# Kernel tuning notes

Hardware: AMD Instinct MI355X
Metric: run time of the kernel (lower is better)

The kernel has to match this reference:

```python
import jax, jax.numpy as jnp
import numpy as np

B, N, D = 2, 2048, 768
H = 12
HD = D // H
HID = 4 * D
SCALE = HD ** -0.5
EPS = 1e-5


def layer_norm(x, g, b):
    mu = jnp.mean(x, axis=-1, keepdims=True)
    var = jnp.var(x, axis=-1, keepdims=True)
    return (x - mu) * jax.lax.rsqrt(var + EPS) * g + b


def setup_inputs() -> dict:
    key = jax.random.key(0)
    ks = jax.random.split(key, 12)
    s = 0.02
    return {
        "x": jax.random.normal(ks[0], (B, N, D), jnp.float32),
        "att_mask": jax.random.randint(ks[1], (B, N), 0, 2, jnp.int32),
        "ln1_g": jnp.ones((D,), jnp.float32),
        "ln1_b": jnp.zeros((D,), jnp.float32),
        "qkv_w": jax.random.normal(ks[2], (3 * D, D), jnp.float32) * s,
        "q_bias": jnp.zeros((D,), jnp.float32),
        "v_bias": jnp.zeros((D,), jnp.float32),
        "proj_w": jax.random.normal(ks[3], (D, D), jnp.float32) * s,
        "proj_b": jnp.zeros((D,), jnp.float32),
        "ln2_g": jnp.ones((D,), jnp.float32),
        "ln2_b": jnp.zeros((D,), jnp.float32),
        "fc1_w": jax.random.normal(ks[4], (HID, D), jnp.float32) * s,
        "fc1_b": jnp.zeros((HID,), jnp.float32),
        "fc2_w": jax.random.normal(ks[5], (D, HID), jnp.float32) * s,
        "fc2_b": jnp.zeros((D,), jnp.float32),
        "gamma_1": 0.1 * jnp.ones((D,), jnp.float32),
        "gamma_2": 0.1 * jnp.ones((D,), jnp.float32),
    }


def reference(x, att_mask, ln1_g, ln1_b, qkv_w, q_bias, v_bias, proj_w, proj_b,
              ln2_g, ln2_b, fc1_w, fc1_b, fc2_w, fc2_b, gamma_1, gamma_2):
    # --- attention branch ---
    h = layer_norm(x, ln1_g, ln1_b)
    qkv_bias = jnp.concatenate([q_bias, jnp.zeros_like(v_bias), v_bias])
    qkv = h @ qkv_w.T + qkv_bias                      # [B,N,3D]
    qkv = qkv.reshape(B, N, 3, H, HD).transpose(2, 0, 3, 1, 4)
    q, k, v = qkv[0], qkv[1], qkv[2]                  # [B,H,N,HD]
    logit = jnp.einsum('bhqd,bhkd->bhqk', q * SCALE, k)
    mask = att_mask[:, None, None, :]                 # key mask [B,1,1,N]
    logit = jnp.where(mask == 0, -jnp.inf, logit)
    attn = jax.nn.softmax(logit, axis=-1)
    o = jnp.einsum('bhqk,bhkd->bhqd', attn, v)
    o = o.transpose(0, 2, 1, 3).reshape(B, N, D)
    o = o @ proj_w.T + proj_b
    x = x + gamma_1 * o
    # --- mlp branch ---
    h2 = layer_norm(x, ln2_g, ln2_b)
    h2 = jax.nn.gelu(h2 @ fc1_w.T + fc1_b, approximate=False)
    h2 = h2 @ fc2_w.T + fc2_b
    return x + gamma_2 * h2
```

## Files before the change

### kernel.cpp

```cpp
#include <hip/hip_runtime.h>
#include <hip/hip_bf16.h>
#include <stdint.h>

typedef __bf16 bf16x8 __attribute__((ext_vector_type(8)));
typedef unsigned short u16x8 __attribute__((ext_vector_type(8)));
typedef float f32x4 __attribute__((ext_vector_type(4)));
typedef float f32x16 __attribute__((ext_vector_type(16)));
typedef uint32_t u32x4 __attribute__((ext_vector_type(4)));

#define DMODEL 768
#define NSEQ   2048
#define BATCH  2
#define NHEAD  12
#define HDIM   64
#define HIDDEN 3072
#define PROWS  (BATCH * NHEAD * NSEQ)
#define QSCALE 0.18033688011112042f

__device__ __forceinline__ uint16_t f2bf(float f) {
  __hip_bfloat16 h = __float2bfloat16(f);
  return __builtin_bit_cast(uint16_t, h);
}
__device__ __forceinline__ float bf2f(uint16_t u) {
  uint32_t x = (uint32_t)u << 16;
  return __builtin_bit_cast(float, x);
}
__device__ __forceinline__ bf16x8 ldb8(const uint16_t* p) {
  return __builtin_bit_cast(bf16x8, *reinterpret_cast<const u16x8*>(p));
}

using as1_void = __attribute__((address_space(1))) const void;
using as3_void = __attribute__((address_space(3))) void;
__device__ __forceinline__ void gload16(const uint16_t* src, uint16_t* lds) {
  __builtin_amdgcn_global_load_lds((as1_void*)src, (as3_void*)lds, 16, 0, 0);
}
#define MEMFENCE asm volatile("" ::: "memory")

#define N_QKVW  (3 * DMODEL * DMODEL)
#define N_PROJW (DMODEL * DMODEL)
#define N_FC1W  (HIDDEN * DMODEL)
#define N_FC2W  (DMODEL * HIDDEN)
__global__ __launch_bounds__(256) void cvt4_kernel(const float* __restrict__ s0,
                                                   const float* __restrict__ s1,
                                                   const float* __restrict__ s2,
                                                   const float* __restrict__ s3,
                                                   uint16_t* __restrict__ d0,
                                                   uint16_t* __restrict__ d1,
                                                   uint16_t* __restrict__ d2,
                                                   uint16_t* __restrict__ d3) {
  int i4 = (blockIdx.x * 256 + threadIdx.x) * 4;
  const float* s;
  uint16_t* d;
  if (i4 < N_QKVW) { s = s0 + i4; d = d0 + i4; }
  else if (i4 < N_QKVW + N_PROJW) { int j = i4 - N_QKVW; s = s1 + j; d = d1 + j; }
  else if (i4 < N_QKVW + N_PROJW + N_FC1W) { int j = i4 - N_QKVW - N_PROJW; s = s2 + j; d = d2 + j; }
  else { int j = i4 - N_QKVW - N_PROJW - N_FC1W; s = s3 + j; d = d3 + j; }
  float4 v = *reinterpret_cast<const float4*>(s);
  ushort4 o;
  o.x = f2bf(v.x); o.y = f2bf(v.y); o.z = f2bf(v.z); o.w = f2bf(v.w);
  *reinterpret_cast<ushort4*>(d) = o;
}

__global__ __launch_bounds__(256) void bias_kernel(const float* __restrict__ qb,
                                                   const float* __restrict__ vb,
                                                   float* __restrict__ out) {
  int j = blockIdx.x * 256 + threadIdx.x;
  if (j < 3 * DMODEL) {
    float v = 0.f;
    if (j < DMODEL) v = qb[j];
    else if (j >= 2 * DMODEL) v = vb[j - 2 * DMODEL];
    out[j] = v;
  }
}

__global__ __launch_bounds__(256) void ln_kernel(const float* __restrict__ x,
                                                 const float* __restrict__ g,
                                                 const float* __restrict__ bt,
                                                 uint16_t* __restrict__ out) {
  const int row = blockIdx.x;
  const int t = threadIdx.x;
  const float* xr = x + (size_t)row * DMODEL;
  float v0 = xr[t], v1 = xr[t + 256], v2 = xr[t + 512];
  float s = v0 + v1 + v2;
  float q = v0 * v0 + v1 * v1 + v2 * v2;
  for (int off = 32; off >= 1; off >>= 1) {
    s += __shfl_xor(s, off);
    q += __shfl_xor(q, off);
  }
  __shared__ float ss[4], sq[4];
  int w = t >> 6;
  if ((t & 63) == 0) { ss[w] = s; sq[w] = q; }
  __syncthreads();
  s = ss[0] + ss[1] + ss[2] + ss[3];
  q = sq[0] + sq[1] + sq[2] + sq[3];
  const float mean = s * (1.0f / DMODEL);
  const float var = q * (1.0f / DMODEL) - mean * mean;
  const float rstd = rsqrtf(var + 1e-5f);
  uint16_t* orow = out + (size_t)row * DMODEL;
  orow[t]       = f2bf((v0 - mean) * rstd * g[t]       + bt[t]);
  orow[t + 256] = f2bf((v1 - mean) * rstd * g[t + 256] + bt[t + 256]);
  orow[t + 512] = f2bf((v2 - mean) * rstd * g[t + 512] + bt[t + 512]);
}

template <int MODE>
__global__ __launch_bounds__(256, 3) void gemm128(const uint16_t* __restrict__ A,
                                                  const uint16_t* __restrict__ W,
                                                  const float* __restrict__ bias,
                                                  void* __restrict__ outp,
                                                  int M, int N, int K) {
  __shared__ uint16_t As[2][128 * 32];
  __shared__ uint16_t Bs[2][128 * 32];
  const int tid = threadIdx.x;
  const int lane = tid & 63;
  const int w = tid >> 6;
  const int wr = w >> 1, wc = w & 1;
  const int row0 = blockIdx.y * 128;
  const int col0 = blockIdx.x * 128;
  const int lr = lane & 15;
  const int g = lane >> 4;

  const int o0 = w * 1024 + lane * 16;
  const int o1 = o0 + 4096;
  const int r0s = o0 >> 6, c0s = (o0 & 63) >> 1;
  const int r1s = o1 >> 6, c1s = (o1 & 63) >> 1;
  const int l0 = (w * 1024) >> 1;
  const int l1 = l0 + 2048;
  const uint16_t* Abase = A + (size_t)row0 * K;
  const uint16_t* Wbase = W + (size_t)col0 * K;

  auto stage = [&](int kt) {
    uint16_t* Ad = &As[kt & 1][0];
    uint16_t* Bd = &Bs[kt & 1][0];
    const int kk = kt * 32;
    gload16(Abase + (size_t)r0s * K + kk + c0s, Ad + l0);
    gload16(Abase + (size_t)r1s * K + kk + c1s, Ad + l1);
    gload16(Wbase + (size_t)r0s * K + kk + c0s, Bd + l0);
    gload16(Wbase + (size_t)r1s * K + kk + c1s, Bd + l1);
  };

  f32x4 acc[4][4] = {};
  const int nt = K >> 5;
  stage(0);
  for (int kt = 0; kt < nt; ++kt) {
    if (kt + 1 < nt) {
      stage(kt + 1);
      asm volatile("s_waitcnt vmcnt(4)" ::: "memory");
    } else {
      asm volatile("s_waitcnt vmcnt(0)" ::: "memory");
    }
    __builtin_amdgcn_s_barrier();
    MEMFENCE;
    const uint16_t* Ab = &As[kt & 1][0];
    const uint16_t* Bb = &Bs[kt & 1][0];
    bf16x8 a[4], b[4];
#pragma unroll
    for (int m = 0; m < 4; ++m) a[m] = ldb8(Ab + (wr * 64 + m * 16 + lr) * 32 + g * 8);
#pragma unroll
    for (int n = 0; n < 4; ++n) b[n] = ldb8(Bb + (wc * 64 + n * 16 + lr) * 32 + g * 8);
#pragma unroll
    for (int m = 0; m < 4; ++m)
#pragma unroll
      for (int n = 0; n < 4; ++n)
        acc[m][n] = __builtin_amdgcn_mfma_f32_16x16x32_bf16(a[m], b[n], acc[m][n], 0, 0, 0);
    MEMFENCE;
    __builtin_amdgcn_s_barrier();
  }

#pragma unroll
  for (int m = 0; m < 4; ++m) {
    int row = row0 + wr * 64 + m * 16 + g * 4;
#pragma unroll
    for (int n = 0; n < 4; ++n) {
      int col = col0 + wc * 64 + n * 16 + lr;
      float bv = bias[col];
#pragma unroll
      for (int ri = 0; ri < 4; ++ri) {
        float val = acc[m][n][ri] + bv;
        size_t idx = (size_t)(row + ri) * N + col;
        if constexpr (MODE == 0) {
          if (col < DMODEL) val *= QSCALE;
          ((uint16_t*)outp)[idx] = f2bf(val);
        } else {
          float ge = 0.5f * val * (1.0f + erff(val * 0.70710678118654752f));
          ((uint16_t*)outp)[idx] = f2bf(ge);
        }
      }
    }
  }
}

__global__ __launch_bounds__(128, 2) void gemm64(const uint16_t* __restrict__ A,
                                                 const uint16_t* __restrict__ W,
                                                 const float* __restrict__ bias,
                                                 float* __restrict__ outp,
                                                 const float* __restrict__ resid,
                                                 const float* __restrict__ gamma,
                                                 int M, int N, int K) {
  __shared__ uint16_t As[2][64 * 32];
  __shared__ uint16_t Bs[2][64 * 32];
  const int tid = threadIdx.x;
  const int lane = tid & 63;
  const int wv = tid >> 6;
  const int row0 = blockIdx.y * 64;
  const int col0 = blockIdx.x * 64;
  const int lr = lane & 15;
  const int g = lane >> 4;
  const int rs = tid >> 2;
  const int cs = (tid & 3) * 8;
  const uint16_t* Abase = A + (size_t)row0 * K;
  const uint16_t* Wbase = W + (size_t)col0 * K;

  auto stage = [&](int kt) {
    uint16_t* Ad = &As[kt & 1][0];
    uint16_t* Bd = &Bs[kt & 1][0];
    const int kk = kt * 32;
#pragma unroll
    for (int i = 0; i < 2; ++i) {
      gload16(Abase + (size_t)(i * 32 + rs) * K + kk + cs, Ad + i * 1024 + wv * 512);
      gload16(Wbase + (size_t)(i * 32 + rs) * K + kk + cs, Bd + i * 1024 + wv * 512);
    }
  };

  f32x4 acc[4][2] = {};
  const int nt = K >> 5;
  stage(0);
  for (int kt = 0; kt < nt; ++kt) {
    if (kt + 1 < nt) {
      stage(kt + 1);
      asm volatile("s_waitcnt vmcnt(4)" ::: "memory");
    } else {
      asm volatile("s_waitcnt vmcnt(0)" ::: "memory");
    }
    __builtin_amdgcn_s_barrier();
    MEMFENCE;
    const uint16_t* Ab = &As[kt & 1][0];
    const uint16_t* Bb = &Bs[kt & 1][0];
    bf16x8 a[4], b[2];
#pragma unroll
    for (int m = 0; m < 4; ++m) a[m] = ldb8(Ab + (m * 16 + lr) * 32 + g * 8);
#pragma unroll
    for (int n = 0; n < 2; ++n) b[n] = ldb8(Bb + (wv * 32 + n * 16 + lr) * 32 + g * 8);
#pragma unroll
    for (int m = 0; m < 4; ++m)
#pragma unroll
      for (int n = 0; n < 2; ++n)
        acc[m][n] = __builtin_amdgcn_mfma_f32_16x16x32_bf16(a[m], b[n], acc[m][n], 0, 0, 0);
    MEMFENCE;
    __builtin_amdgcn_s_barrier();
  }

#pragma unroll
  for (int m = 0; m < 4; ++m) {
    int row = row0 + m * 16 + g * 4;
#pragma unroll
    for (int n = 0; n < 2; ++n) {
      int col = col0 + wv * 32 + n * 16 + lr;
      float bv = bias[col];
      float gv = gamma[col];
#pragma unroll
      for (int ri = 0; ri < 4; ++ri) {
        float val = acc[m][n][ri] + bv;
        size_t idx = (size_t)(row + ri) * N + col;
        outp[idx] = resid[idx] + gv * val;
      }
    }
  }
}

__global__ __launch_bounds__(256) void prep_kernel(const uint16_t* __restrict__ qkv,
                                                   const int* __restrict__ mask,
                                                   uint16_t* __restrict__ km,
                                                   uint16_t* __restrict__ vt) {
  __shared__ uint16_t tile[64][72];
  const int t = threadIdx.x;
  const int bh = blockIdx.x;
  const int n0 = blockIdx.y * 64;
  const int b = bh / NHEAD, h = bh % NHEAD;
  const int* mb = mask + b * NSEQ;
  const uint16_t* src = qkv + (size_t)(b * NSEQ + n0) * (3 * DMODEL) + h * HDIM;
  uint16_t* kdst = km + (size_t)(b * NSEQ + n0) * DMODEL + h * HDIM;
#pragma unroll
  for (int it = 0; it < 2; ++it) {
    int slot = it * 256 + t;
    int r = slot >> 2, c = (slot & 3) * 16;
    uint16_t mz = (mb[n0 + r] != 0) ? (uint16_t)0xFFFF : (uint16_t)0;
    const uint16_t* rp = src + (size_t)r * (3 * DMODEL);
    u16x8 k0 = *reinterpret_cast<const u16x8*>(rp + DMODEL + c) & mz;
    u16x8 k1 = *reinterpret_cast<const u16x8*>(rp + DMODEL + c + 8) & mz;
    u16x8 v0 = *reinterpret_cast<const u16x8*>(rp + 2 * DMODEL + c) & mz;
    u16x8 v1 = *reinterpret_cast<const u16x8*>(rp + 2 * DMODEL + c + 8) & mz;
    *reinterpret_cast<u16x8*>(kdst + (size_t)r * DMODEL + c) = k0;
    *reinterpret_cast<u16x8*>(kdst + (size_t)r * DMODEL + c + 8) = k1;
    *reinterpret_cast<u16x8*>(&tile[r][c]) = v0;
    *reinterpret_cast<u16x8*>(&tile[r][c + 8]) = v1;
  }
  __syncthreads();
  uint16_t* dst = vt + (size_t)bh * HDIM * NSEQ + n0;
#pragma unroll
  for (int it = 0; it < 2; ++it) {
    int slot = it * 256 + t;
    int d = slot >> 2, c = (slot & 3) * 16;
    u16x8 a0, a1;
#pragma unroll
    for (int e = 0; e < 8; ++e) a0[e] = tile[c + e][d];
#pragma unroll
    for (int e = 0; e < 8; ++e) a1[e] = tile[c + 8 + e][d];
    *reinterpret_cast<u16x8*>(dst + (size_t)d * NSEQ + c) = a0;
    *reinterpret_cast<u16x8*>(dst + (size_t)d * NSEQ + c + 8) = a1;
  }
}

__global__ __launch_bounds__(256, 3) void attn_kernel(const uint16_t* __restrict__ qkv,
                                                      const uint16_t* __restrict__ km,
                                                      const uint16_t* __restrict__ vt,
                                                      const int* __restrict__ mask,
                                                      uint16_t* __restrict__ po,
                                                      float* __restrict__ pml) {
  __shared__ uint16_t Kb[2][64 * 64];
  __shared__ uint16_t Vb[2][64 * 64];
  __shared__ unsigned long long mbits[16];
  const int tid = threadIdx.x;
  const int lane = tid & 63;
  const int w = tid >> 6;
  const int bh = blockIdx.x;
  const int b = bh / NHEAD, hd = bh % NHEAD;
  const int z = blockIdx.z;
  const int kbase = z * 1024;
  const int q0 = blockIdx.y * 128 + w * 32;
  const int l31 = lane & 31;
  const int hh = lane >> 5;

  const int* mb = mask + b * NSEQ;
#pragma unroll
  for (int it = 0; it < 4; ++it) {
    unsigned long long bm = __ballot(mb[kbase + it * 256 + tid] != 0);
    if (lane == 0) mbits[it * 4 + w] = bm;
  }

  bf16x8 qa[4];
  const uint16_t* qptr = qkv + (size_t)(b * NSEQ + q0 + l31) * (3 * DMODEL) + hd * HDIM + hh * 8;
#pragma unroll
  for (int dblk = 0; dblk < 4; ++dblk) qa[dblk] = ldb8(qptr + dblk * 16);

  const uint16_t* kmb = km + (size_t)b * NSEQ * DMODEL + hd * HDIM;
  const uint16_t* vtb = vt + (size_t)bh * HDIM * NSEQ;

  __syncthreads();

  const int srow = tid >> 3;
  const int sxor = ((tid & 7) ^ (srow & 7)) * 8;
  auto stage = [&](int t) {
    const int pb = t & 1;
    const int k0 = kbase + t * 64;
#pragma unroll
    for (int i = 0; i < 2; ++i) {
      const int row = i * 32 + srow;
      gload16(kmb + (size_t)(k0 + row) * DMODEL + sxor, &Kb[pb][i * 2048 + w * 512]);
      gload16(vtb + (size_t)row * NSEQ + k0 + sxor, &Vb[pb][i * 2048 + w * 512]);
    }
  };

  float m_ = 0.f, lsum = 0.f;
  f32x16 oacc[2] = {};

  stage(0);
  for (int t = 0; t < 16; ++t) {
    if (t + 1 < 16) {
      stage(t + 1);
      asm volatile("s_waitcnt vmcnt(4)" ::: "memory");
    } else {
      asm volatile("s_waitcnt vmcnt(0)" ::: "memory");
    }
    __builtin_amdgcn_s_barrier();
    MEMFENCE;
    const uint16_t* Kbp = &Kb[t & 1][0];
    const uint16_t* Vbp = &Vb[t & 1][0];

    f32x16 st[2];
    __builtin_amdgcn_s_setprio(1);
#pragma unroll
    for (int kblk = 0; kblk < 2; ++kblk) {
      f32x16 acc = {};
      const uint16_t* kr = Kbp + (kblk * 32 + l31) * 64;
#pragma unroll
      for (int dblk = 0; dblk < 4; ++dblk) {
        bf16x8 kf = ldb8(kr + ((dblk * 2 + hh) ^ (l31 & 7)) * 8);
        acc = __builtin_amdgcn_mfma_f32_32x32x16_bf16(kf, qa[dblk], acc, 0, 0, 0);
      }
      st[kblk] = acc;
    }
    __builtin_amdgcn_s_setprio(0);

    float tm = -1e30f;
#pragma unroll
    for (int kblk = 0; kblk < 2; ++kblk)
#pragma unroll
      for (int r = 0; r < 16; ++r) tm = fmaxf(tm, st[kblk][r]);
    tm = fmaxf(tm, __shfl_xor(tm, 32));
    if (__any(tm - m_ > 16.0f)) {
      float mn = fmaxf(m_, tm);
      float al = exp2f(m_ - mn);
      lsum *= al;
      m_ = mn;
      float ar[16];
#pragma unroll
      for (int r = 0; r < 16; ++r)
        ar[r] = __shfl(al, (r & 3) + 8 * (r >> 2) + 4 * hh);
#pragma unroll
      for (int dblk = 0; dblk < 2; ++dblk)
#pragma unroll
        for (int r = 0; r < 16; ++r) oacc[dblk][r] *= ar[r];
    }

    float ls = 0.f;
    uint32_t pk[2][8];
#pragma unroll
    for (int kblk = 0; kblk < 2; ++kblk)
#pragma unroll
      for (int wn = 0; wn < 8; ++wn) {
        float e0 = exp2f(st[kblk][2 * wn] - m_);
        float e1 = exp2f(st[kblk][2 * wn + 1] - m_);
        ls += e0 + e1;
        pk[kblk][wn] = (uint32_t)f2bf(e0) | ((uint32_t)f2bf(e1) << 16);
      }
    ls += __shfl_xor(ls, 32);
    const unsigned long long wb = mbits[t];
    const float cnt = (float)(64 - __popcll(wb));
    ls -= cnt * exp2f(0.f - m_);
    lsum += ls;

    bf16x8 af[4];
#pragma unroll
    for (int kb16 = 0; kb16 < 4; ++kb16) {
      const int kblk = kb16 >> 1;
      const int a4 = (kb16 & 1) * 4;
      uint32_t ow0 = hh ? pk[kblk][a4 + 2] : pk[kblk][a4 + 0];
      uint32_t ow1 = hh ? pk[kblk][a4 + 3] : pk[kblk][a4 + 1];
      uint32_t gv0 = hh ? pk[kblk][a4 + 0] : pk[kblk][a4 + 2];
      uint32_t gv1 = hh ? pk[kblk][a4 + 1] : pk[kblk][a4 + 3];
      uint32_t sw0 = (uint32_t)__shfl_xor((int)gv0, 32);
      uint32_t sw1 = (uint32_t)__shfl_xor((int)gv1, 32);
      u32x4 afu;
      afu[0] = hh ? sw0 : ow0;
      afu[1] = hh ? sw1 : ow1;
      afu[2] = hh ? ow0 : sw0;
      afu[3] = hh ? ow1 : sw1;
      af[kb16] = __builtin_bit_cast(bf16x8, afu);
    }

    __builtin_amdgcn_s_setprio(1);
#pragma unroll
    for (int dblk = 0; dblk < 2; ++dblk) {
      const uint16_t* vr = Vbp + (dblk * 32 + l31) * 64;
#pragma unroll
      for (int kb16 = 0; kb16 < 4; ++kb16) {
        bf16x8 vf = ldb8(vr + ((kb16 * 2 + hh) ^ (l31 & 7)) * 8);
        oacc[dblk] = __builtin_amdgcn_mfma_f32_32x32x16_bf16(af[kb16], vf, oacc[dblk], 0, 0, 0);
      }
    }
    __builtin_amdgcn_s_setprio(0);
    MEMFENCE;
    __builtin_amdgcn_s_barrier();
  }

  uint16_t* ob = po + ((size_t)z * PROWS + (size_t)bh * NSEQ + q0) * 64;
#pragma unroll
  for (int r = 0; r < 16; ++r) {
    const int qrow = (r & 3) + 8 * (r >> 2) + 4 * hh;
#pragma unroll
    for (int dblk = 0; dblk < 2; ++dblk)
      ob[(size_t)qrow * 64 + dblk * 32 + l31] = f2bf(oacc[dblk][r]);
  }
  if (hh == 0) {
    float2* pp = (float2*)(pml + ((size_t)z * PROWS + (size_t)bh * NSEQ + q0 + l31) * 2);
    *pp = make_float2(m_, lsum);
  }
}

__global__ __launch_bounds__(256) void merge_kernel(const uint16_t* __restrict__ po,
                                                    const float* __restrict__ pml,
                                                    uint16_t* __restrict__ o) {
  int gid = blockIdx.x * 256 + threadIdx.x;
  int row = gid >> 3;
  int c0 = (gid & 7) * 8;
  float m1 = pml[(size_t)row * 2], l1 = pml[(size_t)row * 2 + 1];
  float m2 = pml[((size_t)PROWS + row) * 2], l2 = pml[((size_t)PROWS + row) * 2 + 1];
  float M = fmaxf(m1, m2);
  float w1 = exp2f(m1 - M), w2 = exp2f(m2 - M);
  float L = w1 * l1 + w2 * l2;
  float inv = L > 0.f ? 1.f / L : 0.f;
  w1 *= inv; w2 *= inv;
  u16x8 a = *reinterpret_cast<const u16x8*>(po + (size_t)row * 64 + c0);
  u16x8 b = *reinterpret_cast<const u16x8*>(po + ((size_t)PROWS + row) * 64 + c0);
  int bh = row >> 11, q = row & 2047;
  int bb = bh / NHEAD, hh = bh % NHEAD;
  uint16_t* op = o + ((size_t)(bb * NSEQ + q) * DMODEL + hh * HDIM + c0);
  u16x8 outv;
#pragma unroll
  for (int e = 0; e < 8; ++e)
    outv[e] = f2bf(w1 * bf2f(a[e]) + w2 * bf2f(b[e]));
  *reinterpret_cast<u16x8*>(op) = outv;
}

extern "C" void kernel_launch(void* const* d_in, const int* in_sizes, int n_in,
                              void* d_out, int out_size, void* d_ws, size_t ws_size,
                              hipStream_t stream) {
  const float* x      = (const float*)d_in[0];
  const int*   amask  = (const int*)d_in[1];
  const float* ln1_g  = (const float*)d_in[2];
  const float* ln1_b  = (const float*)d_in[3];
  const float* qkv_w  = (const float*)d_in[4];
  const float* q_bias = (const float*)d_in[5];
  const float* v_bias = (const float*)d_in[6];
  const float* proj_w = (const float*)d_in[7];
  const float* proj_b = (const float*)d_in[8];
  const float* ln2_g  = (const float*)d_in[9];
  const float* ln2_b  = (const float*)d_in[10];
  const float* fc1_w  = (const float*)d_in[11];
  const float* fc1_b  = (const float*)d_in[12];
  const float* fc2_w  = (const float*)d_in[13];
  const float* fc2_b  = (const float*)d_in[14];
  const float* g1     = (const float*)d_in[15];
  const float* g2     = (const float*)d_in[16];

  char* ws = (char*)d_ws;
  uint16_t* qkvw_bf  = (uint16_t*)(ws + 0);
  uint16_t* projw_bf = (uint16_t*)(ws + 3538944);
  uint16_t* fc1w_bf  = (uint16_t*)(ws + 4718592);
  uint16_t* fc2w_bf  = (uint16_t*)(ws + 9437184);
  float*    qkvbias  = (float*)(ws + 14155776);
  uint16_t* h_bf     = (uint16_t*)(ws + 14164992);
  uint16_t* km       = h_bf;
  uint16_t* h2_bf    = h_bf;
  uint16_t* qkv_bf   = (uint16_t*)(ws + 20456448);
  uint16_t* vt_bf    = (uint16_t*)(ws + 39330816);
  uint16_t* o_bf     = (uint16_t*)(ws + 45622272);
  float*    x1_f     = (float*)(ws + 51913728);
  uint16_t* po       = (uint16_t*)(ws + 51913728);
  float*    pml      = (float*)(ws + 64496640);
  uint16_t* fc1_bf   = qkv_bf;

  const int M = BATCH * NSEQ;

  cvt4_kernel<<<(N_QKVW + N_PROJW + N_FC1W + N_FC2W) / 1024, 256, 0, stream>>>(
      qkv_w, proj_w, fc1_w, fc2_w, qkvw_bf, projw_bf, fc1w_bf, fc2w_bf);
  bias_kernel<<<(3 * DMODEL + 255) / 256, 256, 0, stream>>>(q_bias, v_bias, qkvbias);

  ln_kernel<<<M, 256, 0, stream>>>(x, ln1_g, ln1_b, h_bf);
  gemm128<0><<<dim3((3 * DMODEL) / 128, M / 128), 256, 0, stream>>>(
      h_bf, qkvw_bf, qkvbias, qkv_bf, M, 3 * DMODEL, DMODEL);
  prep_kernel<<<dim3(BATCH * NHEAD, NSEQ / 64), 256, 0, stream>>>(qkv_bf, amask, km, vt_bf);
  attn_kernel<<<dim3(BATCH * NHEAD, NSEQ / 128, 2), 256, 0, stream>>>(
      qkv_bf, km, vt_bf, amask, po, pml);
  merge_kernel<<<(PROWS * 8) / 256, 256, 0, stream>>>(po, pml, o_bf);
  gemm64<<<dim3(DMODEL / 64, M / 64), 128, 0, stream>>>(
      o_bf, projw_bf, proj_b, x1_f, x, g1, M, DMODEL, DMODEL);
  ln_kernel<<<M, 256, 0, stream>>>(x1_f, ln2_g, ln2_b, h2_bf);
  gemm128<2><<<dim3(HIDDEN / 128, M / 128), 256, 0, stream>>>(
      h2_bf, fc1w_bf, fc1_b, fc1_bf, M, HIDDEN, DMODEL);
  gemm64<<<dim3(DMODEL / 64, M / 64), 128, 0, stream>>>(
      fc1_bf, fc2w_bf, fc2_b, (float*)d_out, x1_f, g2, M, DMODEL, HIDDEN);
}
```

Measured before the change: 222.2 us.

## Restructure gemm64 to 4 waves with K=64 swizzled tiles; compute softmax rowsum via MFMA

The 64x64 output GEMM now uses 256 threads (a 2x2 wave grid) with a K tile of 64 and XOR-swizzled shared-memory rows, which halves the number of loop iterations and barriers and aims to reduce LDS bank conflicts. Separately, the attention kernel stops summing softmax probabilities with scalar adds and cross-lane shuffles. It instead accumulates the row sums with an extra MFMA against a vector of ones and applies the mask correction at the end. This adds MFMA work and a per-row shuffle epilogue, and the row sum is now taken from the bf16-rounded probabilities.

```diff
diff --git a/kernel.cpp b/kernel.cpp
--- a/kernel.cpp
+++ b/kernel.cpp
@@ -189,40 +189,44 @@
   }
 }
 
-__global__ __launch_bounds__(128, 2) void gemm64(const uint16_t* __restrict__ A,
+__global__ __launch_bounds__(256, 3) void gemm64(const uint16_t* __restrict__ A,
                                                  const uint16_t* __restrict__ W,
                                                  const float* __restrict__ bias,
                                                  float* __restrict__ outp,
                                                  const float* __restrict__ resid,
                                                  const float* __restrict__ gamma,
                                                  int M, int N, int K) {
-  __shared__ uint16_t As[2][64 * 32];
-  __shared__ uint16_t Bs[2][64 * 32];
+  __shared__ uint16_t As[2][64 * 64];
+  __shared__ uint16_t Bs[2][64 * 64];
   const int tid = threadIdx.x;
   const int lane = tid & 63;
-  const int wv = tid >> 6;
+  const int w = tid >> 6;
+  const int wr = w >> 1, wc = w & 1;
   const int row0 = blockIdx.y * 64;
   const int col0 = blockIdx.x * 64;
   const int lr = lane & 15;
   const int g = lane >> 4;
-  const int rs = tid >> 2;
-  const int cs = (tid & 3) * 8;
+
+  const int srow = tid >> 3;
+  const int schunk = tid & 7;
   const uint16_t* Abase = A + (size_t)row0 * K;
   const uint16_t* Wbase = W + (size_t)col0 * K;
 
   auto stage = [&](int kt) {
     uint16_t* Ad = &As[kt & 1][0];
     uint16_t* Bd = &Bs[kt & 1][0];
-    const int kk = kt * 32;
+    const int kk = kt * 64;
 #pragma unroll
     for (int i = 0; i < 2; ++i) {
-      gload16(Abase + (size_t)(i * 32 + rs) * K + kk + cs, Ad + i * 1024 + wv * 512);
-      gload16(Wbase + (size_t)(i * 32 + rs) * K + kk + cs, Bd + i * 1024 + wv * 512);
+      const int row = i * 32 + srow;
+      const int sc = (schunk ^ (row & 7)) * 8;
+      gload16(Abase + (size_t)row * K + kk + sc, Ad + i * 2048 + w * 512);
+      gload16(Wbase + (size_t)row * K + kk + sc, Bd + i * 2048 + w * 512);
     }
   };
 
-  f32x4 acc[4][2] = {};
-  const int nt = K >> 5;
+  f32x4 acc[2][2] = {};
+  const int nt = K >> 6;
   stage(0);
   for (int kt = 0; kt < nt; ++kt) {
     if (kt + 1 < nt) {
@@ -235,26 +239,35 @@
     MEMFENCE;
     const uint16_t* Ab = &As[kt & 1][0];
     const uint16_t* Bb = &Bs[kt & 1][0];
-    bf16x8 a[4], b[2];
-#pragma unroll
-    for (int m = 0; m < 4; ++m) a[m] = ldb8(Ab + (m * 16 + lr) * 32 + g * 8);
-#pragma unroll
-    for (int n = 0; n < 2; ++n) b[n] = ldb8(Bb + (wv * 32 + n * 16 + lr) * 32 + g * 8);
-#pragma unroll
-    for (int m = 0; m < 4; ++m)
-#pragma unroll
-      for (int n = 0; n < 2; ++n)
-        acc[m][n] = __builtin_amdgcn_mfma_f32_16x16x32_bf16(a[m], b[n], acc[m][n], 0, 0, 0);
+#pragma unroll
+    for (int kk = 0; kk < 2; ++kk) {
+      bf16x8 a[2], bf[2];
+#pragma unroll
+      for (int m = 0; m < 2; ++m) {
+        const int row = wr * 32 + m * 16 + lr;
+        a[m] = ldb8(Ab + row * 64 + (((kk * 4 + g) ^ (row & 7)) * 8));
+      }
+#pragma unroll
+      for (int n = 0; n < 2; ++n) {
+        const int row = wc * 32 + n * 16 + lr;
+        bf[n] = ldb8(Bb + row * 64 + (((kk * 4 + g) ^ (row & 7)) * 8));
+      }
+#pragma unroll
+      for (int m = 0; m < 2; ++m)
+#pragma unroll
+        for (int n = 0; n < 2; ++n)
+          acc[m][n] = __builtin_amdgcn_mfma_f32_16x16x32_bf16(a[m], bf[n], acc[m][n], 0, 0, 0);
+    }
     MEMFENCE;
     __builtin_amdgcn_s_barrier();
   }
 
 #pragma unroll
-  for (int m = 0; m < 4; ++m) {
-    int row = row0 + m * 16 + g * 4;
+  for (int m = 0; m < 2; ++m) {
+    int row = row0 + wr * 32 + m * 16 + g * 4;
 #pragma unroll
     for (int n = 0; n < 2; ++n) {
-      int col = col0 + wv * 32 + n * 16 + lr;
+      int col = col0 + wc * 32 + n * 16 + lr;
       float bv = bias[col];
       float gv = gamma[col];
 #pragma unroll
@@ -360,8 +373,14 @@
     }
   };
 
-  float m_ = 0.f, lsum = 0.f;
+  u16x8 ones_u;
+#pragma unroll
+  for (int e = 0; e < 8; ++e) ones_u[e] = 0x3F80;
+  const bf16x8 ones = __builtin_bit_cast(bf16x8, ones_u);
+
+  float m_ = 0.f, corr = 0.f;
   f32x16 oacc[2] = {};
+  f32x16 lacc = {};
 
   stage(0);
   for (int t = 0; t < 16; ++t) {
@@ -391,28 +410,29 @@
     }
     __builtin_amdgcn_s_setprio(0);
 
-    float tm = -1e30f;
-#pragma unroll
-    for (int kblk = 0; kblk < 2; ++kblk)
-#pragma unroll
-      for (int r = 0; r < 16; ++r) tm = fmaxf(tm, st[kblk][r]);
+    float tm = fmaxf(st[0][0], st[0][1]);
+#pragma unroll
+    for (int r = 2; r < 16; r += 2) tm = fmaxf(fmaxf(tm, st[0][r]), st[0][r + 1]);
+#pragma unroll
+    for (int r = 0; r < 16; r += 2) tm = fmaxf(fmaxf(tm, st[1][r]), st[1][r + 1]);
     tm = fmaxf(tm, __shfl_xor(tm, 32));
     if (__any(tm - m_ > 16.0f)) {
       float mn = fmaxf(m_, tm);
       float al = exp2f(m_ - mn);
-      lsum *= al;
+      corr *= al;
       m_ = mn;
       float ar[16];
 #pragma unroll
       for (int r = 0; r < 16; ++r)
         ar[r] = __shfl(al, (r & 3) + 8 * (r >> 2) + 4 * hh);
 #pragma unroll
-      for (int dblk = 0; dblk < 2; ++dblk)
-#pragma unroll
-        for (int r = 0; r < 16; ++r) oacc[dblk][r] *= ar[r];
-    }
-
-    float ls = 0.f;
+      for (int r = 0; r < 16; ++r) {
+        oacc[0][r] *= ar[r];
+        oacc[1][r] *= ar[r];
+        lacc[r] *= ar[r];
+      }
+    }
+
     uint32_t pk[2][8];
 #pragma unroll
     for (int kblk = 0; kblk < 2; ++kblk)
@@ -420,14 +440,10 @@
       for (int wn = 0; wn < 8; ++wn) {
         float e0 = exp2f(st[kblk][2 * wn] - m_);
         float e1 = exp2f(st[kblk][2 * wn + 1] - m_);
-        ls += e0 + e1;
         pk[kblk][wn] = (uint32_t)f2bf(e0) | ((uint32_t)f2bf(e1) << 16);
       }
-    ls += __shfl_xor(ls, 32);
     const unsigned long long wb = mbits[t];
-    const float cnt = (float)(64 - __popcll(wb));
-    ls -= cnt * exp2f(0.f - m_);
-    lsum += ls;
+    corr += (float)(64 - __popcll(wb)) * exp2f(0.f - m_);
 
     bf16x8 af[4];
 #pragma unroll
@@ -458,6 +474,9 @@
         oacc[dblk] = __builtin_amdgcn_mfma_f32_32x32x16_bf16(af[kb16], vf, oacc[dblk], 0, 0, 0);
       }
     }
+#pragma unroll
+    for (int kb16 = 0; kb16 < 4; ++kb16)
+      lacc = __builtin_amdgcn_mfma_f32_32x32x16_bf16(af[kb16], ones, lacc, 0, 0, 0);
     __builtin_amdgcn_s_setprio(0);
     MEMFENCE;
     __builtin_amdgcn_s_barrier();
@@ -471,9 +490,15 @@
     for (int dblk = 0; dblk < 2; ++dblk)
       ob[(size_t)qrow * 64 + dblk * 32 + l31] = f2bf(oacc[dblk][r]);
   }
-  if (hh == 0) {
-    float2* pp = (float2*)(pml + ((size_t)z * PROWS + (size_t)bh * NSEQ + q0 + l31) * 2);
-    *pp = make_float2(m_, lsum);
+#pragma unroll
+  for (int r = 0; r < 16; ++r) {
+    const int qrow = (r & 3) + 8 * (r >> 2) + 4 * hh;
+    float mr = __shfl(m_, qrow);
+    float cr = __shfl(corr, qrow);
+    float dr = lacc[r] - cr;
+    if (l31 == 0)
+      *(float2*)(pml + ((size_t)z * PROWS + (size_t)bh * NSEQ + q0 + qrow) * 2) =
+          make_float2(mr, dr);
   }
 }
 
@@ -553,11 +578,11 @@
   attn_kernel<<<dim3(BATCH * NHEAD, NSEQ / 128, 2), 256, 0, stream>>>(
       qkv_bf, km, vt_bf, amask, po, pml);
   merge_kernel<<<(PROWS * 8) / 256, 256, 0, stream>>>(po, pml, o_bf);
-  gemm64<<<dim3(DMODEL / 64, M / 64), 128, 0, stream>>>(
+  gemm64<<<dim3(DMODEL / 64, M / 64), 256, 0, stream>>>(
       o_bf, projw_bf, proj_b, x1_f, x, g1, M, DMODEL, DMODEL);
   ln_kernel<<<M, 256, 0, stream>>>(x1_f, ln2_g, ln2_b, h2_bf);
   gemm128<2><<<dim3(HIDDEN / 128, M / 128), 256, 0, stream>>>(
       h2_bf, fc1w_bf, fc1_b, fc1_bf, M, HIDDEN, DMODEL);
-  gemm64<<<dim3(DMODEL / 64, M / 64), 128, 0, stream>>>(
+  gemm64<<<dim3(DMODEL / 64, M / 64), 256, 0, stream>>>(
       fc1_bf, fc2w_bf, fc2_b, (float*)d_out, x1_f, g2, M, DMODEL, HIDDEN);
 }
```

Measured after the change: 202.7 us. 1.1x faster.
